# Kernel tuning notes

Measured on AMD Instinct MI355X. Metric: run time of the kernel, lower is better.

## Reference

```python
import jax, jax.numpy as jnp
import numpy as np

N_HEADS = 16
D_EMB = 1024
D_HEAD = D_EMB // N_HEADS


def setup_inputs() -> dict:
    key = jax.random.key(0)
    ks = jax.random.split(key, 5)
    scale = 1.0 / np.sqrt(D_EMB)
    x = jax.random.normal(ks[0], (4, 2048, D_EMB), dtype=jnp.float32)
    W_in = jax.random.normal(ks[1], (3 * D_EMB, D_EMB), dtype=jnp.float32) * scale
    b_in = jax.random.normal(ks[2], (3 * D_EMB,), dtype=jnp.float32) * 0.01
    W_out = jax.random.normal(ks[3], (D_EMB, D_EMB), dtype=jnp.float32) * scale
    b_out = jax.random.normal(ks[4], (D_EMB,), dtype=jnp.float32) * 0.01
    return {"x": x, "W_in": W_in, "b_in": b_in, "W_out": W_out, "b_out": b_out}


def reference(x, W_in, b_in, W_out, b_out):
    b, s, d = x.shape
    qkv = x @ W_in.T + b_in  # [b, s, 3d]
    q, k, v = jnp.split(qkv, 3, axis=-1)
    def heads(t):
        return t.reshape(b, s, N_HEADS, D_HEAD).transpose(0, 2, 1, 3)  # [b,h,s,dh]
    q, k, v = heads(q), heads(k), heads(v)
    scores = jnp.einsum('bhqd,bhkd->bhqk', q, k)
    causal = jnp.tril(jnp.ones((s, s), dtype=bool))  # keep lower-triangular incl diag
    scores = jnp.where(causal, scores, -jnp.inf)
    scores = scores / np.sqrt(D_HEAD).astype(np.float32)
    w = jax.nn.softmax(scores, axis=-1)
    out = jnp.einsum('bhqk,bhkd->bhqd', w, v)  # [b,h,s,dh]
    out = out.transpose(0, 2, 1, 3).reshape(b, s, d)
    return out @ W_out.T + b_out
```

## Files before the change

### kernel.cpp

```cpp
#include <hip/hip_runtime.h>
#include <hip/hip_bf16.h>
#include <cstdint>


typedef float  floatx4  __attribute__((ext_vector_type(4)));
typedef __bf16 bf16x8   __attribute__((ext_vector_type(8)));
typedef __bf16 bf16x4   __attribute__((ext_vector_type(4)));
typedef short  shortx4  __attribute__((ext_vector_type(4)));
typedef unsigned int   uint32x2 __attribute__((ext_vector_type(2)));
typedef unsigned short ushortx8 __attribute__((ext_vector_type(8)));

#define MFMA16(a,b,c) __builtin_amdgcn_mfma_f32_16x16x32_bf16(a, b, c, 0, 0, 0)

__device__ __forceinline__ floatx4 mfma_k16(bf16x4 a, bf16x4 b, floatx4 c) {
#if defined(__HIP_DEVICE_COMPILE__)
#if __has_builtin(__builtin_amdgcn_mfma_f32_16x16x16_bf16)
  return __builtin_amdgcn_mfma_f32_16x16x16_bf16(a, b, c, 0, 0, 0);
#elif __has_builtin(__builtin_amdgcn_mfma_f32_16x16x16bf16_1k)
  return __builtin_amdgcn_mfma_f32_16x16x16bf16_1k(
      __builtin_bit_cast(shortx4, a), __builtin_bit_cast(shortx4, b), c, 0, 0, 0);
#else
  floatx4 d;
  asm("v_mfma_f32_16x16x16_bf16 %0, %1, %2, %3"
      : "=v"(d)
      : "v"(__builtin_bit_cast(uint32x2, a)),
        "v"(__builtin_bit_cast(uint32x2, b)), "v"(c));
  return d;
#endif
#else
  (void)a; (void)b;
  return c;
#endif
}

__device__ __forceinline__ float fast_exp2(float x) {
#if defined(__HIP_DEVICE_COMPILE__)
#if __has_builtin(__builtin_amdgcn_exp2f)
  return __builtin_amdgcn_exp2f(x);
#else
  float r;
  asm("v_exp_f32 %0, %1" : "=v"(r) : "v"(x));
  return r;
#endif
#else
  return x;
#endif
}

#define C_SCALE 0.18033688011112042f

__device__ __forceinline__ void gload_lds16(const void* g, void* l) {
  __builtin_amdgcn_global_load_lds(
      (__attribute__((address_space(1))) void*)(g),
      (__attribute__((address_space(3))) void*)(l), 16, 0, 0);
}

#define N_X4    2097152
#define N_WIN4  786432
#define N_WOUT4 262144
#define N_B4    768
__global__ __launch_bounds__(256) void cast_fused(
    const float* __restrict__ x, const float* __restrict__ W_in,
    const float* __restrict__ W_out, const float* __restrict__ b_in,
    __bf16* __restrict__ xb, __bf16* __restrict__ Winb,
    __bf16* __restrict__ Woutb, float* __restrict__ bins) {
  int i = blockIdx.x * 256 + threadIdx.x;
  if (i < N_X4) {
    const float4 v = ((const float4*)x)[i];
    bf16x4 o;
    o.x = (__bf16)v.x; o.y = (__bf16)v.y; o.z = (__bf16)v.z; o.w = (__bf16)v.w;
    ((bf16x4*)xb)[i] = o;
  } else if (i < N_X4 + N_WIN4) {
    const int j = i - N_X4;
    const float s = (j < 262144) ? C_SCALE : 1.0f;
    const float4 v = ((const float4*)W_in)[j];
    bf16x4 o;
    o.x = (__bf16)(v.x * s); o.y = (__bf16)(v.y * s);
    o.z = (__bf16)(v.z * s); o.w = (__bf16)(v.w * s);
    ((bf16x4*)Winb)[j] = o;
  } else if (i < N_X4 + N_WIN4 + N_WOUT4) {
    const int j = i - N_X4 - N_WIN4;
    const float4 v = ((const float4*)W_out)[j];
    bf16x4 o;
    o.x = (__bf16)v.x; o.y = (__bf16)v.y; o.z = (__bf16)v.z; o.w = (__bf16)v.w;
    ((bf16x4*)Woutb)[j] = o;
  } else {
    const int j = i - N_X4 - N_WIN4 - N_WOUT4;
    const float s = (j < 256) ? C_SCALE : 1.0f;
    float4 v = ((const float4*)b_in)[j];
    v.x *= s; v.y *= s; v.z *= s; v.w *= s;
    ((float4*)bins)[j] = v;
  }
}

template <int MODE>
__global__ __launch_bounds__(256) void gemm_bt(
    const __bf16* __restrict__ A, const __bf16* __restrict__ B,
    const float* __restrict__ bias, void* __restrict__ Cout,
    __bf16* __restrict__ Vt, int M, int N, int K) {
  __shared__ __bf16 As[128 * 64];
  __shared__ __bf16 Bs[128 * 64];
  const int tid = threadIdx.x;
  const int wave = tid >> 6, lane = tid & 63;
  const int quad = lane >> 4, l15 = lane & 15;
  const int wm = (wave & 1) * 64, wn = (wave >> 1) * 64;

  const int nwg = (int)(gridDim.x * gridDim.y);
  int f = (int)(blockIdx.y * gridDim.x + blockIdx.x);
  f = (f & 7) * (nwg >> 3) + (f >> 3);
  const int bx = f % (int)gridDim.x;
  const int by = f / (int)gridDim.x;
  const long row0 = (long)by * 128;
  const long col0 = (long)bx * 128;

  floatx4 acc[4][4] = {};

  const int sr = tid >> 3;
  const int swz = 8 * ((tid & 7) ^ (sr & 7));
  const __bf16* ga = A + (row0 + sr) * (long)K + swz;
  const __bf16* gb = B + (col0 + sr) * (long)K + swz;
  __bf16* lA = As + tid * 8;
  __bf16* lB = Bs + tid * 8;
  const int rswz = (l15 & 7) * 8;

  for (int k0 = 0; k0 < K; k0 += 64) {
#pragma unroll
    for (int c = 0; c < 4; ++c) {
      gload_lds16(ga + (long)(32 * c) * K, lA + c * 2048);
      gload_lds16(gb + (long)(32 * c) * K, lB + c * 2048);
    }
    ga += 64; gb += 64;
    __syncthreads();

#pragma unroll
    for (int kh = 0; kh < 2; ++kh) {
      const int kc = (kh * 32 + quad * 8) ^ rswz;
      bf16x8 af[4], bfr[4];
#pragma unroll
      for (int i = 0; i < 4; ++i)
        af[i] = *(const bf16x8*)(As + (wm + i * 16 + l15) * 64 + kc);
#pragma unroll
      for (int j = 0; j < 4; ++j)
        bfr[j] = *(const bf16x8*)(Bs + (wn + j * 16 + l15) * 64 + kc);
#pragma unroll
      for (int i = 0; i < 4; ++i)
#pragma unroll
        for (int j = 0; j < 4; ++j)
          acc[i][j] = MFMA16(af[i], bfr[j], acc[i][j]);
    }
    __syncthreads();
  }

#pragma unroll
  for (int i = 0; i < 4; ++i) {
    const long r0 = row0 + wm + i * 16 + quad * 4;
#pragma unroll
    for (int j = 0; j < 4; ++j) {
      const long c = col0 + wn + j * 16 + l15;
      const float bv = bias[c];
      if (MODE == 0) {
#pragma unroll
        for (int reg = 0; reg < 4; ++reg)
          ((float*)Cout)[(r0 + reg) * (long)N + c] = acc[i][j][reg] + bv;
      } else {
        if (c < 2048) {
#pragma unroll
          for (int reg = 0; reg < 4; ++reg)
            ((__bf16*)Cout)[(r0 + reg) * (long)N + c] =
                (__bf16)(acc[i][j][reg] + bv);
        } else {
          const int cc = (int)c - 2048;
          const int hh = cc >> 6, dh = cc & 63;
          const int bb = (int)(r0 >> 11), s = (int)(r0 & 2047);
          bf16x4 pk;
#pragma unroll
          for (int reg = 0; reg < 4; ++reg)
            pk[reg] = (__bf16)(acc[i][j][reg] + bv);
          *(bf16x4*)(Vt + ((long)(bb * 16 + hh) * 64 + dh) * 2048 + s) = pk;
        }
      }
    }
  }
}

__global__ __launch_bounds__(256, 2) void flash_attn(
    const __bf16* __restrict__ qkv,
    const __bf16* __restrict__ Vt,
    __bf16* __restrict__ Out) {
  constexpr int S = 2048;
  const int h = blockIdx.y, b = blockIdx.z;
  const int x = (int)(blockIdx.x + 5 * blockIdx.z + 3 * blockIdx.y) & 7;
  const int qt0 = x, qt1 = 15 - x, qt2 = 16 + x, qt3 = 31 - x;
  const int km0 = x + 1, km1 = 16 - x, km2 = 17 + x;
  const int kmax = 32 - x;

  __shared__ __bf16 Ks[2][64 * 72];
  __shared__ __bf16 Vs[2][64 * 72];

  const int tid = threadIdx.x, wave = tid >> 6, lane = tid & 63;
  const int quad = lane >> 4, l15 = lane & 15;

  bf16x8 qf[4][2];
  {
    const int qts[4] = {qt0, qt1, qt2, qt3};
#pragma unroll
    for (int s = 0; s < 4; ++s) {
      const long qr = (long)(b * S + qts[s] * 64 + wave * 16 + l15) * 3072 + h * 64;
      qf[s][0] = *(const bf16x8*)(qkv + qr + quad * 8);
      qf[s][1] = *(const bf16x8*)(qkv + qr + 32 + quad * 8);
    }
  }

  bf16x4 ones4;
#pragma unroll
  for (int j = 0; j < 4; ++j) ones4[j] = (__bf16)1.0f;

  floatx4 o[4][4] = {};
  floatx4 ldn[4] = {};

  const int srow = tid >> 3;
  const int sc8 = (tid & 7) * 8;
  const __bf16* ka = qkv + ((long)(b * S) + srow) * 3072 + 1024 + h * 64 + sc8;
  const __bf16* va = Vt + ((long)(b * 16 + h) * 64 + srow) * S + sc8;
  const int sl = srow * 72 + sc8;

  ushortx8 kr0 = *(const ushortx8*)ka;
  ushortx8 kr1 = *(const ushortx8*)(ka + 32 * 3072);
  ushortx8 vr0 = *(const ushortx8*)va;
  ushortx8 vr1 = *(const ushortx8*)(va + 32 * (long)S);
  *(ushortx8*)(&Ks[0][sl]) = kr0;
  *(ushortx8*)(&Ks[0][sl + 32 * 72]) = kr1;
  *(ushortx8*)(&Vs[0][sl]) = vr0;
  *(ushortx8*)(&Vs[0][sl + 32 * 72]) = vr1;
  kr0 = *(const ushortx8*)(ka + 64 * 3072);
  kr1 = *(const ushortx8*)(ka + 96 * 3072);
  vr0 = *(const ushortx8*)(va + 64);
  vr1 = *(const ushortx8*)(va + 32 * (long)S + 64);
  const __bf16* kn = ka + 128 * 3072;
  const __bf16* vn = va + 128;
  __syncthreads();

  for (int kt = 0; kt < kmax; ++kt) {
    const int cur = kt & 1;
    if (kt + 1 < kmax) {
      *(ushortx8*)(&Ks[cur ^ 1][sl]) = kr0;
      *(ushortx8*)(&Ks[cur ^ 1][sl + 32 * 72]) = kr1;
      *(ushortx8*)(&Vs[cur ^ 1][sl]) = vr0;
      *(ushortx8*)(&Vs[cur ^ 1][sl + 32 * 72]) = vr1;
    }
    if (kt + 2 < kmax) {
      kr0 = *(const ushortx8*)kn;
      kr1 = *(const ushortx8*)(kn + 32 * 3072);
      vr0 = *(const ushortx8*)vn;
      vr1 = *(const ushortx8*)(vn + 32 * (long)S);
      kn += 64 * 3072; vn += 64;
    }

    const bool a0 = kt < km0;
    const bool a1 = kt < km1;
    const bool a2 = kt < km2;
    const int qts[4] = {qt0, qt1, qt2, qt3};

    bf16x4 pf[4][4];
#pragma unroll
    for (int nb = 0; nb < 4; ++nb) {
      const bf16x8 k0 = *(const bf16x8*)(&Ks[cur][(nb * 16 + l15) * 72 + quad * 8]);
      const bf16x8 k1 = *(const bf16x8*)(&Ks[cur][(nb * 16 + l15) * 72 + 32 + quad * 8]);
      const int key0 = kt * 64 + nb * 16 + quad * 4;
#pragma unroll
      for (int s = 0; s < 4; ++s) {
        const bool act = (s == 0) ? a0 : (s == 1) ? a1 : (s == 2) ? a2 : true;
        if (act) {
          floatx4 z = {0.f, 0.f, 0.f, 0.f};
          z = MFMA16(k0, qf[s][0], z);
          z = MFMA16(k1, qf[s][1], z);
          if (kt == qts[s]) {
            const int qg = qts[s] * 64 + wave * 16 + l15;
#pragma unroll
            for (int r = 0; r < 4; ++r)
              if (key0 + r > qg) z[r] = -1.0e30f;
          }
#pragma unroll
          for (int r = 0; r < 4; ++r)
            pf[s][nb][r] = (__bf16)fast_exp2(z[r]);
        }
      }
    }

#pragma unroll
    for (int c = 0; c < 4; ++c) {
      if (a0) ldn[0] = mfma_k16(ones4, pf[0][c], ldn[0]);
      if (a1) ldn[1] = mfma_k16(ones4, pf[1][c], ldn[1]);
      if (a2) ldn[2] = mfma_k16(ones4, pf[2][c], ldn[2]);
      ldn[3] = mfma_k16(ones4, pf[3][c], ldn[3]);
    }

    __builtin_amdgcn_s_setprio(1);
#pragma unroll
    for (int mb = 0; mb < 4; ++mb) {
#pragma unroll
      for (int c = 0; c < 4; ++c) {
        const bf16x4 vf = *(const bf16x4*)(&Vs[cur][(mb * 16 + l15) * 72 + c * 16 + quad * 4]);
        if (a0) o[0][mb] = mfma_k16(vf, pf[0][c], o[0][mb]);
        if (a1) o[1][mb] = mfma_k16(vf, pf[1][c], o[1][mb]);
        if (a2) o[2][mb] = mfma_k16(vf, pf[2][c], o[2][mb]);
        o[3][mb] = mfma_k16(vf, pf[3][c], o[3][mb]);
      }
    }
    __builtin_amdgcn_s_setprio(0);
    __syncthreads();
  }

  {
    const int qts[4] = {qt0, qt1, qt2, qt3};
#pragma unroll
    for (int s = 0; s < 4; ++s) {
      const float inv = 1.f / ldn[s][0];
      const long row = (long)(b * S + qts[s] * 64 + wave * 16 + l15);
#pragma unroll
      for (int mb = 0; mb < 4; ++mb) {
        bf16x4 pk;
#pragma unroll
        for (int r = 0; r < 4; ++r) pk[r] = (__bf16)(o[s][mb][r] * inv);
        *(bf16x4*)(Out + row * 1024 + h * 64 + mb * 16 + quad * 4) = pk;
      }
    }
  }
}

extern "C" void kernel_launch(void* const* d_in, const int* in_sizes, int n_in,
                              void* d_out, int out_size, void* d_ws, size_t ws_size,
                              hipStream_t stream) {
  const float* x     = (const float*)d_in[0];
  const float* W_in  = (const float*)d_in[1];
  const float* b_in  = (const float*)d_in[2];
  const float* W_out = (const float*)d_in[3];
  const float* b_out = (const float*)d_in[4];

  const int BS = 4 * 2048;
  const int D = 1024, N3 = 3072;

  char* w = (char*)d_ws;
  __bf16* xb    = (__bf16*)w;  w += (size_t)BS * D * 2;
  __bf16* Winb  = (__bf16*)w;  w += (size_t)N3 * D * 2;
  __bf16* Woutb = (__bf16*)w;  w += (size_t)D * D * 2;
  __bf16* qkvb  = (__bf16*)w;  w += (size_t)BS * N3 * 2;
  __bf16* Vtb   = (__bf16*)w;  w += (size_t)64 * 64 * 2048 * 2;
  __bf16* attnb = (__bf16*)w;  w += (size_t)BS * D * 2;
  float*  bins  = (float*)w;   w += (size_t)N3 * 4;

  const int castN = N_X4 + N_WIN4 + N_WOUT4 + N_B4;
  cast_fused<<<dim3(castN / 256), 256, 0, stream>>>(
      x, W_in, W_out, b_in, xb, Winb, Woutb, bins);

  gemm_bt<2><<<dim3(N3 / 128, BS / 128), 256, 0, stream>>>(
      xb, Winb, bins, (void*)qkvb, Vtb, BS, N3, D);

  flash_attn<<<dim3(8, 16, 4), 256, 0, stream>>>(qkvb, Vtb, attnb);

  gemm_bt<0><<<dim3(D / 128, BS / 128), 256, 0, stream>>>(
      attnb, Woutb, b_out, d_out, nullptr, BS, D, D);
}
```

Baseline: 282.2 us.

## Split flash attention into one query tile per block with 32-key tiles

Each attention block now handles a single 64-row query tile instead of four load-balanced tiles, so the grid grows from 8x16x4 to 32x16x4 blocks. Key tiles shrink to 32 keys and shared memory is smaller, which allows higher occupancy through launch bounds of 8. The aim is more parallelism and lower register pressure, at the cost of losing K/V reuse across four query tiles, reloading K/V per tile, and uneven causal work across blocks.

```diff
diff --git a/kernel.cpp b/kernel.cpp
--- a/kernel.cpp
+++ b/kernel.cpp
@@ -183,128 +183,97 @@
   }
 }
 
-__global__ __launch_bounds__(256, 2) void flash_attn(
+__global__ __launch_bounds__(256, 8) void flash_attn(
     const __bf16* __restrict__ qkv,
     const __bf16* __restrict__ Vt,
     __bf16* __restrict__ Out) {
   constexpr int S = 2048;
   const int h = blockIdx.y, b = blockIdx.z;
-  const int x = (int)(blockIdx.x + 5 * blockIdx.z + 3 * blockIdx.y) & 7;
-  const int qt0 = x, qt1 = 15 - x, qt2 = 16 + x, qt3 = 31 - x;
-  const int km0 = x + 1, km1 = 16 - x, km2 = 17 + x;
-  const int kmax = 32 - x;
-
-  __shared__ __bf16 Ks[2][64 * 72];
-  __shared__ __bf16 Vs[2][64 * 72];
+  const int qt = (int)(blockIdx.x + 5 * blockIdx.z + 3 * blockIdx.y) & 31;
+  const int nk = 2 * (qt + 1);
+
+  __shared__ __bf16 Ks[2][32 * 72];
+  __shared__ __bf16 Vs[2][64 * 36];
 
   const int tid = threadIdx.x, wave = tid >> 6, lane = tid & 63;
   const int quad = lane >> 4, l15 = lane & 15;
 
-  bf16x8 qf[4][2];
+  bf16x8 qf0, qf1;
   {
-    const int qts[4] = {qt0, qt1, qt2, qt3};
-#pragma unroll
-    for (int s = 0; s < 4; ++s) {
-      const long qr = (long)(b * S + qts[s] * 64 + wave * 16 + l15) * 3072 + h * 64;
-      qf[s][0] = *(const bf16x8*)(qkv + qr + quad * 8);
-      qf[s][1] = *(const bf16x8*)(qkv + qr + 32 + quad * 8);
-    }
+    const long qr = (long)(b * S + qt * 64 + wave * 16 + l15) * 3072 + h * 64;
+    qf0 = *(const bf16x8*)(qkv + qr + quad * 8);
+    qf1 = *(const bf16x8*)(qkv + qr + 32 + quad * 8);
   }
 
   bf16x4 ones4;
 #pragma unroll
   for (int j = 0; j < 4; ++j) ones4[j] = (__bf16)1.0f;
 
-  floatx4 o[4][4] = {};
-  floatx4 ldn[4] = {};
-
-  const int srow = tid >> 3;
-  const int sc8 = (tid & 7) * 8;
+  floatx4 oA[4] = {};
+  floatx4 lA = {0.f, 0.f, 0.f, 0.f};
+
+  const int srow = tid >> 3, sc8 = (tid & 7) * 8;
+  const int vd = tid >> 2,  vc8 = (tid & 3) * 8;
   const __bf16* ka = qkv + ((long)(b * S) + srow) * 3072 + 1024 + h * 64 + sc8;
-  const __bf16* va = Vt + ((long)(b * 16 + h) * 64 + srow) * S + sc8;
-  const int sl = srow * 72 + sc8;
-
-  ushortx8 kr0 = *(const ushortx8*)ka;
-  ushortx8 kr1 = *(const ushortx8*)(ka + 32 * 3072);
-  ushortx8 vr0 = *(const ushortx8*)va;
-  ushortx8 vr1 = *(const ushortx8*)(va + 32 * (long)S);
-  *(ushortx8*)(&Ks[0][sl]) = kr0;
-  *(ushortx8*)(&Ks[0][sl + 32 * 72]) = kr1;
-  *(ushortx8*)(&Vs[0][sl]) = vr0;
-  *(ushortx8*)(&Vs[0][sl + 32 * 72]) = vr1;
-  kr0 = *(const ushortx8*)(ka + 64 * 3072);
-  kr1 = *(const ushortx8*)(ka + 96 * 3072);
-  vr0 = *(const ushortx8*)(va + 64);
-  vr1 = *(const ushortx8*)(va + 32 * (long)S + 64);
-  const __bf16* kn = ka + 128 * 3072;
-  const __bf16* vn = va + 128;
+  const __bf16* va = Vt + ((long)(b * 16 + h) * 64 + vd) * S + vc8;
+  const int slk = srow * 72 + sc8;
+  const int slv = vd * 36 + vc8;
+
+  ushortx8 kr = *(const ushortx8*)ka;
+  ushortx8 vr = *(const ushortx8*)va;
+  *(ushortx8*)(&Ks[0][slk]) = kr;
+  *(ushortx8*)(&Vs[0][slv]) = vr;
+  kr = *(const ushortx8*)(ka + 32 * 3072);
+  vr = *(const ushortx8*)(va + 32);
+  const __bf16* kn = ka + 64 * 3072;
+  const __bf16* vn = va + 64;
   __syncthreads();
 
-  for (int kt = 0; kt < kmax; ++kt) {
+  const int qg = qt * 64 + wave * 16 + l15;
+  const int wall = qt << 1;
+
+  for (int kt = 0; kt < nk; ++kt) {
     const int cur = kt & 1;
-    if (kt + 1 < kmax) {
-      *(ushortx8*)(&Ks[cur ^ 1][sl]) = kr0;
-      *(ushortx8*)(&Ks[cur ^ 1][sl + 32 * 72]) = kr1;
-      *(ushortx8*)(&Vs[cur ^ 1][sl]) = vr0;
-      *(ushortx8*)(&Vs[cur ^ 1][sl + 32 * 72]) = vr1;
-    }
-    if (kt + 2 < kmax) {
-      kr0 = *(const ushortx8*)kn;
-      kr1 = *(const ushortx8*)(kn + 32 * 3072);
-      vr0 = *(const ushortx8*)vn;
-      vr1 = *(const ushortx8*)(vn + 32 * (long)S);
-      kn += 64 * 3072; vn += 64;
-    }
-
-    const bool a0 = kt < km0;
-    const bool a1 = kt < km1;
-    const bool a2 = kt < km2;
-    const int qts[4] = {qt0, qt1, qt2, qt3};
-
-    bf16x4 pf[4][4];
-#pragma unroll
-    for (int nb = 0; nb < 4; ++nb) {
-      const bf16x8 k0 = *(const bf16x8*)(&Ks[cur][(nb * 16 + l15) * 72 + quad * 8]);
-      const bf16x8 k1 = *(const bf16x8*)(&Ks[cur][(nb * 16 + l15) * 72 + 32 + quad * 8]);
-      const int key0 = kt * 64 + nb * 16 + quad * 4;
-#pragma unroll
-      for (int s = 0; s < 4; ++s) {
-        const bool act = (s == 0) ? a0 : (s == 1) ? a1 : (s == 2) ? a2 : true;
-        if (act) {
-          floatx4 z = {0.f, 0.f, 0.f, 0.f};
-          z = MFMA16(k0, qf[s][0], z);
-          z = MFMA16(k1, qf[s][1], z);
-          if (kt == qts[s]) {
-            const int qg = qts[s] * 64 + wave * 16 + l15;
-#pragma unroll
-            for (int r = 0; r < 4; ++r)
-              if (key0 + r > qg) z[r] = -1.0e30f;
-          }
-#pragma unroll
-          for (int r = 0; r < 4; ++r)
-            pf[s][nb][r] = (__bf16)fast_exp2(z[r]);
-        }
+    if (kt + 1 < nk) {
+      *(ushortx8*)(&Ks[cur ^ 1][slk]) = kr;
+      *(ushortx8*)(&Vs[cur ^ 1][slv]) = vr;
+    }
+    if (kt + 2 < nk) {
+      kr = *(const ushortx8*)kn;
+      vr = *(const ushortx8*)vn;
+      kn += 32 * 3072; vn += 32;
+    }
+
+    bf16x4 pf[2];
+    __builtin_amdgcn_s_setprio(1);
+#pragma unroll
+    for (int nb = 0; nb < 2; ++nb) {
+      const int krow = (nb * 16 + l15) * 72;
+      const bf16x8 k0 = *(const bf16x8*)(&Ks[cur][krow + quad * 8]);
+      const bf16x8 k1 = *(const bf16x8*)(&Ks[cur][krow + 32 + quad * 8]);
+      floatx4 z = {0.f, 0.f, 0.f, 0.f};
+      z = MFMA16(k0, qf0, z);
+      z = MFMA16(k1, qf1, z);
+      if (kt >= wall) {
+        const int key0 = kt * 32 + nb * 16 + quad * 4;
+#pragma unroll
+        for (int r = 0; r < 4; ++r)
+          if (key0 + r > qg) z[r] = -1.0e30f;
       }
-    }
-
-#pragma unroll
-    for (int c = 0; c < 4; ++c) {
-      if (a0) ldn[0] = mfma_k16(ones4, pf[0][c], ldn[0]);
-      if (a1) ldn[1] = mfma_k16(ones4, pf[1][c], ldn[1]);
-      if (a2) ldn[2] = mfma_k16(ones4, pf[2][c], ldn[2]);
-      ldn[3] = mfma_k16(ones4, pf[3][c], ldn[3]);
-    }
-
-    __builtin_amdgcn_s_setprio(1);
+#pragma unroll
+      for (int r = 0; r < 4; ++r)
+        pf[nb][r] = (__bf16)fast_exp2(z[r]);
+    }
+    lA = mfma_k16(ones4, pf[0], lA);
+    lA = mfma_k16(ones4, pf[1], lA);
+
 #pragma unroll
     for (int mb = 0; mb < 4; ++mb) {
-#pragma unroll
-      for (int c = 0; c < 4; ++c) {
-        const bf16x4 vf = *(const bf16x4*)(&Vs[cur][(mb * 16 + l15) * 72 + c * 16 + quad * 4]);
-        if (a0) o[0][mb] = mfma_k16(vf, pf[0][c], o[0][mb]);
-        if (a1) o[1][mb] = mfma_k16(vf, pf[1][c], o[1][mb]);
-        if (a2) o[2][mb] = mfma_k16(vf, pf[2][c], o[2][mb]);
-        o[3][mb] = mfma_k16(vf, pf[3][c], o[3][mb]);
+      const int vrow = (mb * 16 + l15) * 36;
+#pragma unroll
+      for (int c = 0; c < 2; ++c) {
+        const bf16x4 vf = *(const bf16x4*)(&Vs[cur][vrow + c * 16 + quad * 4]);
+        oA[mb] = mfma_k16(vf, pf[c], oA[mb]);
       }
     }
     __builtin_amdgcn_s_setprio(0);
@@ -312,18 +281,14 @@
   }
 
   {
-    const int qts[4] = {qt0, qt1, qt2, qt3};
-#pragma unroll
-    for (int s = 0; s < 4; ++s) {
-      const float inv = 1.f / ldn[s][0];
-      const long row = (long)(b * S + qts[s] * 64 + wave * 16 + l15);
-#pragma unroll
-      for (int mb = 0; mb < 4; ++mb) {
-        bf16x4 pk;
-#pragma unroll
-        for (int r = 0; r < 4; ++r) pk[r] = (__bf16)(o[s][mb][r] * inv);
-        *(bf16x4*)(Out + row * 1024 + h * 64 + mb * 16 + quad * 4) = pk;
-      }
+    const float inv = 1.f / lA[0];
+    const long row = (long)(b * S + qt * 64 + wave * 16 + l15);
+#pragma unroll
+    for (int mb = 0; mb < 4; ++mb) {
+      bf16x4 pk;
+#pragma unroll
+      for (int r = 0; r < 4; ++r) pk[r] = (__bf16)(oA[mb][r] * inv);
+      *(bf16x4*)(Out + row * 1024 + h * 64 + mb * 16 + quad * 4) = pk;
     }
   }
 }
@@ -356,7 +321,7 @@
   gemm_bt<2><<<dim3(N3 / 128, BS / 128), 256, 0, stream>>>(
       xb, Winb, bins, (void*)qkvb, Vtb, BS, N3, D);
 
-  flash_attn<<<dim3(8, 16, 4), 256, 0, stream>>>(qkvb, Vtb, attnb);
+  flash_attn<<<dim3(32, 16, 4), 256, 0, stream>>>(qkvb, Vtb, attnb);
 
   gemm_bt<0><<<dim3(D / 128, BS / 128), 256, 0, stream>>>(
       attnb, Woutb, b_out, d_out, nullptr, BS, D, D);
```

Result: faster. 271.2 us (-3.9%).
